# Kernel tuning notes

Measured on AMD Instinct MI355X. Metric: run time of the kernel, lower is better.

## Reference

```python
import jax, jax.numpy as jnp
import numpy as np

# dims: batch, samples, agents, obs_dim, action_dim, hidden
B, S, N, D, A, H = 512, 64, 8, 64, 16, 256
IN_DIM = (D + A) * N  # 640


def mish(x):
    return x * jnp.tanh(jax.nn.softplus(x))


def setup_inputs() -> dict:
    key = jax.random.key(0)
    ks = jax.random.split(key, 9)
    u = lambda k, shape, fan_in: jax.random.uniform(
        k, shape, jnp.float32, -1.0 / np.sqrt(fan_in), 1.0 / np.sqrt(fan_in))
    return {
        "state": jax.random.normal(ks[0], (B, N, D), jnp.float32),
        "action": jax.random.normal(ks[1], (B, N, A), jnp.float32),
        "W1": u(ks[2], (IN_DIM, H), IN_DIM),
        "b1": u(ks[3], (H,), IN_DIM),
        "W2": u(ks[4], (H, H), H),
        "b2": u(ks[5], (H,), H),
        "W3": u(ks[6], (H, 1), H),
        "b3": u(ks[7], (1,), H),
        # random grand-coalition permutations of the N agents, per (batch, sample)
        "perm": jnp.argsort(jax.random.uniform(ks[8], (B, S, N)), axis=-1).astype(jnp.int32),
    }


def reference(state, action, W1, b1, W2, b2, W3, b3, perm):
    # subcoalition mask [B,S,N,N]: torch builds one-hot(perm) @ tril(ones),
    # i.e. mask[b,s,i,j] = 1 iff j <= perm[b,s,i]
    subcoal = (jnp.arange(N) <= perm[..., None]).astype(state.dtype)
    # gathered actions in coalition order [B,S,N,A]: act_g[b,s,j] = action[b, perm[b,s,j]]
    act_g = action[jnp.arange(B)[:, None, None], perm]
    # masked subcoalition actions [B,S,N,N,A] -> [B,S,N,N*A]
    act = (act_g[:, :, None, :, :] * subcoal[..., None]).reshape(B, S, N, N * A)
    # flattened global obs broadcast over (sample, agent) axes [B,S,N,N*D]
    obs = jnp.broadcast_to(state.reshape(B, 1, 1, N * D), (B, S, N, N * D))
    x = jnp.concatenate([obs, act], axis=-1)  # [B,S,N,IN_DIM]
    # per-agent loop in torch uses shared q1 weights -> single batched MLP
    h = mish(x @ W1 + b1)
    h = mish(h @ W2 + b2)
    q = h @ W3 + b3                   # [B,S,N,1]
    q1 = q.mean(axis=1).squeeze(-1)   # mean over samples -> [B,N]
    return (q1, q1)
```

## Files before the change

kernel.cpp:

```cpp
#include <hip/hip_runtime.h>
#include <hip/hip_bf16.h>

typedef unsigned short ushort_t;
typedef __attribute__((ext_vector_type(8))) short short8;
typedef __attribute__((ext_vector_type(4))) float floatx4;


__device__ __forceinline__ float mish_f(float x) {
    float e = __expf(x);
    float w = fmaf(e, e + 2.0f, 2.0f);
    return x - 2.0f * x * __builtin_amdgcn_rcpf(w);
}

__device__ __forceinline__ unsigned f2bf_u(float f) {
    return (__float_as_uint(f) + 0x8000u) >> 16;
}

__device__ __forceinline__ unsigned pk_bf2(float a, float b) {
    unsigned ua = __float_as_uint(a) + 0x8000u;
    unsigned ub = __float_as_uint(b) + 0x8000u;
#if __has_builtin(__builtin_amdgcn_perm)
    return __builtin_amdgcn_perm(ua, ub, 0x03020706u);
#else
    return (ua >> 16) | (ub & 0xffff0000u);
#endif
}

__global__ __launch_bounds__(256) void prep_kernel(
        const float* __restrict__ state,
        const float* __restrict__ action,
        const float* __restrict__ W1,
        const float* __restrict__ b1,
        const float* __restrict__ W2,
        float* __restrict__ obsW,
        ushort_t* __restrict__ actW,
        ushort_t* __restrict__ W2T) {
    int bid = blockIdx.x;
    int t = threadIdx.x;
    if (bid < 512) {
        int b = bid;
        const float* stp = state + (size_t)b * 512;
        const float* w1p = W1 + t;
        float a0 = 0.f, a1 = 0.f, a2 = 0.f, a3 = 0.f;
#pragma unroll 8
        for (int f = 0; f < 512; f += 4) {
            a0 = fmaf(stp[f + 0], w1p[(f + 0) * 256], a0);
            a1 = fmaf(stp[f + 1], w1p[(f + 1) * 256], a1);
            a2 = fmaf(stp[f + 2], w1p[(f + 2) * 256], a2);
            a3 = fmaf(stp[f + 3], w1p[(f + 3) * 256], a3);
        }
        obsW[b * 256 + t] = (a0 + a1) + (a2 + a3) + b1[t];
    } else if (bid < 1536) {
        int idx = bid - 512;
        int j = idx & 7;
        int b0 = (idx >> 3) * 4;
        const float* W1a = W1 + (size_t)(512 + j * 16) * 256;
        float wv[16];
#pragma unroll
        for (int a = 0; a < 16; ++a) wv[a] = W1a[a * 256 + t];
#pragma unroll
        for (int bb = 0; bb < 4; ++bb) {
            int b = b0 + bb;
            const float* acp = action + (size_t)b * 128;
            float acc[8];
#pragma unroll
            for (int n = 0; n < 8; ++n) acc[n] = 0.f;
#pragma unroll
            for (int a = 0; a < 16; ++a) {
#pragma unroll
                for (int n = 0; n < 8; ++n)
                    acc[n] = fmaf(acp[n * 16 + a], wv[a], acc[n]);
            }
#pragma unroll
            for (int n = 0; n < 8; ++n)
                actW[(((size_t)b * 8 + n) * 8 + j) * 256 + t] = (ushort_t)f2bf_u(acc[n]);
        }
    } else {
        int n = (bid - 1536) * 4 + (t >> 6);
        int klo = (t & 63);
        for (int kk = 0; kk < 4; ++kk) {
            int k = kk * 64 + klo;
            W2T[n * 256 + k] = (ushort_t)f2bf_u(W2[k * 256 + n]);
        }
    }
}

#define CHUNK_US 528

__global__ __launch_bounds__(512, 4) void main_kernel(
        const float* __restrict__ obsW, const ushort_t* __restrict__ actW,
        const ushort_t* __restrict__ W2T, const int* __restrict__ perm,
        const float* __restrict__ b2,
        const float* __restrict__ W3, const float* __restrict__ b3,
        float* __restrict__ out) {
    __shared__ __align__(16) ushort_t h1[32 * CHUNK_US];
    __shared__ __align__(16) float obsb[256];
    __shared__ int perm_s[64];
    __shared__ float qpart[8][64];
    __shared__ float qv_s[64];

    int t = threadIdx.x;
    int bid = blockIdx.x;
    int b = (bid & 7) * 64 + ((bid >> 3) & 63);
    int sg = bid >> 9;
    int s0 = sg * 8;

    int w = t >> 6;
    int L = t & 63;
    int lo = L & 15;
    int q = L >> 4;

    if (t < 256) obsb[t] = obsW[b * 256 + t];
    else if (t < 320) perm_s[t - 256] = perm[((size_t)b * 64 + s0) * 8 + (t - 256)];

    const ushort_t* w2base = W2T + ((size_t)(w * 32 + lo)) * 256 + q * 8;
    short8 bpre[4];
    bpre[0] = *reinterpret_cast<const short8*>(w2base + 0 * 16 * 256 + 0 * 32);
    bpre[1] = *reinterpret_cast<const short8*>(w2base + 1 * 16 * 256 + 0 * 32);
    bpre[2] = *reinterpret_cast<const short8*>(w2base + 0 * 16 * 256 + 1 * 32);
    bpre[3] = *reinterpret_cast<const short8*>(w2base + 1 * 16 * 256 + 1 * 32);

    __syncthreads();

    {
        int sl = w;
        int hg = L;
        int g = hg >> 1;
        int ks = g >> 2;
        int qq = g & 3;
        int half = hg & 1;
        const ushort_t* actg = actW + (size_t)b * 64 * 256 + hg * 4;
        uint2 av[8];
#pragma unroll
        for (int j = 0; j < 8; ++j) {
            int p = perm_s[sl * 8 + j];
            av[j] = *reinterpret_cast<const uint2*>(actg + (p * 8 + j) * 256);
        }
        float4 ob = *reinterpret_cast<const float4*>(obsb + hg * 4);
        float r0 = ob.x, r1 = ob.y, r2 = ob.z, r3 = ob.w;
        ushort_t* dst0 = h1 + (qq * 16) * 8 + half * 4 + ks * CHUNK_US;
#pragma unroll
        for (int j = 0; j < 8; ++j) {
            r0 += __uint_as_float(av[j].x << 16);
            r1 += __uint_as_float(av[j].x & 0xffff0000u);
            r2 += __uint_as_float(av[j].y << 16);
            r3 += __uint_as_float(av[j].y & 0xffff0000u);
            int row = sl * 8 + j;
            int mt = row >> 4, lr = row & 15;
            uint2 pk = make_uint2(pk_bf2(mish_f(r0), mish_f(r1)),
                                  pk_bf2(mish_f(r2), mish_f(r3)));
            *reinterpret_cast<uint2*>(dst0 + mt * 8 * CHUNK_US + lr * 8) = pk;
        }
    }
    __syncthreads();

    floatx4 acc[4][2];
#pragma unroll
    for (int mt = 0; mt < 4; ++mt)
#pragma unroll
        for (int nt = 0; nt < 2; ++nt)
            acc[mt][nt] = (floatx4){0.f, 0.f, 0.f, 0.f};

    const ushort_t* h1b = h1 + L * 8;

#pragma unroll
    for (int ks = 0; ks < 8; ++ks) {
        short8 afr[4];
#pragma unroll
        for (int mt = 0; mt < 4; ++mt)
            afr[mt] = *reinterpret_cast<const short8*>(h1b + (mt * 8 + ks) * CHUNK_US);
#pragma unroll
        for (int nt = 0; nt < 2; ++nt) {
            short8 bfr;
            if (ks == 0)      bfr = bpre[nt];
            else if (ks == 1) bfr = bpre[2 + nt];
            else              bfr = *reinterpret_cast<const short8*>(w2base + nt * 16 * 256 + ks * 32);
#pragma unroll
            for (int mt = 0; mt < 4; ++mt)
                acc[mt][nt] = __builtin_amdgcn_mfma_f32_16x16x32_bf16(afr[mt], bfr, acc[mt][nt], 0, 0, 0);
        }
    }

    float b2c[2], w3c[2];
#pragma unroll
    for (int nt = 0; nt < 2; ++nt) {
        int col = w * 32 + nt * 16 + lo;
        b2c[nt] = b2[col];
        w3c[nt] = W3[col];
    }
#pragma unroll
    for (int mt = 0; mt < 4; ++mt) {
        float part[4] = {0.f, 0.f, 0.f, 0.f};
#pragma unroll
        for (int nt = 0; nt < 2; ++nt) {
#pragma unroll
            for (int r = 0; r < 4; ++r) {
                float h2 = mish_f(acc[mt][nt][r] + b2c[nt]);
                part[r] = fmaf(h2, w3c[nt], part[r]);
            }
        }
#pragma unroll
        for (int r = 0; r < 4; ++r) {
            float v = part[r];
            v += __shfl_xor(v, 1);
            v += __shfl_xor(v, 2);
            v += __shfl_xor(v, 4);
            v += __shfl_xor(v, 8);
            if (lo == 0) qpart[w][mt * 16 + q * 4 + r] = v;
        }
    }
    __syncthreads();
    if (t < 64) {
        float qv = b3[0];
#pragma unroll
        for (int ww = 0; ww < 8; ++ww) qv += qpart[ww][t];
        qv_s[t] = qv;
    }
    __syncthreads();
    if (t < 8) {
        float p = 0.f;
#pragma unroll
        for (int sl = 0; sl < 8; ++sl)
            p += qv_s[sl * 8 + perm_s[sl * 8 + t]];
        p *= (1.0f / 64.0f);
        atomicAdd(&out[b * 8 + t], p);
        atomicAdd(&out[4096 + b * 8 + t], p);
    }
}

extern "C" void kernel_launch(void* const* d_in, const int* in_sizes, int n_in,
                              void* d_out, int out_size, void* d_ws, size_t ws_size,
                              hipStream_t stream) {
    const float* state  = (const float*)d_in[0];
    const float* action = (const float*)d_in[1];
    const float* W1     = (const float*)d_in[2];
    const float* b1     = (const float*)d_in[3];
    const float* W2     = (const float*)d_in[4];
    const float* b2     = (const float*)d_in[5];
    const float* W3     = (const float*)d_in[6];
    const float* b3     = (const float*)d_in[7];
    const int*   perm   = (const int*)d_in[8];
    float* out = (float*)d_out;

    char* ws = (char*)d_ws;
    float*    obsW = (float*)ws;
    ushort_t* actW = (ushort_t*)(ws + 524288);
    ushort_t* W2T  = (ushort_t*)(ws + 524288 + 16777216);

    (void)hipMemsetAsync(out, 0, (size_t)out_size * sizeof(float), stream);
    prep_kernel<<<1600, 256, 0, stream>>>(state, action, W1, b1, W2, obsW, actW, W2T);
    main_kernel<<<4096, 512, 0, stream>>>(obsW, actW, W2T, perm, b2, W3, b3, out);
}
```

Measured before the change: 184.4 us.

## Switch to fp16 MFMA with exp2-prescaled mish, DPP reductions, fused output zeroing

Intermediates and W2 are now stored as fp16 instead of bf16, and the layer-2 matmul uses f16 MFMA. Pre-activations are pre-scaled by log2(e) so mish can use exp2 directly in a packed float2 form. The W3 dot product uses fdot2 and the 16-lane reductions use DPP instead of shuffles. The output memset is folded into the prep kernel and the prep grid is rebalanced. fp16 has narrower range than bf16, which could overflow, and fp16 rounding of h2 and W3 adds error.

```diff
diff --git a/kernel.cpp b/kernel.cpp
--- a/kernel.cpp
+++ b/kernel.cpp
@@ -2,28 +2,49 @@
 #include <hip/hip_bf16.h>
 
 typedef unsigned short ushort_t;
-typedef __attribute__((ext_vector_type(8))) short short8;
+typedef _Float16 half_t;
+typedef __attribute__((ext_vector_type(2))) _Float16 half2_t;
+typedef __attribute__((ext_vector_type(8))) _Float16 half8_t;
+typedef __attribute__((ext_vector_type(2))) float fx2;
 typedef __attribute__((ext_vector_type(4))) float floatx4;
 
-
-__device__ __forceinline__ float mish_f(float x) {
-    float e = __expf(x);
-    float w = fmaf(e, e + 2.0f, 2.0f);
-    return x - 2.0f * x * __builtin_amdgcn_rcpf(w);
-}
-
-__device__ __forceinline__ unsigned f2bf_u(float f) {
-    return (__float_as_uint(f) + 0x8000u) >> 16;
-}
-
-__device__ __forceinline__ unsigned pk_bf2(float a, float b) {
-    unsigned ua = __float_as_uint(a) + 0x8000u;
-    unsigned ub = __float_as_uint(b) + 0x8000u;
-#if __has_builtin(__builtin_amdgcn_perm)
-    return __builtin_amdgcn_perm(ua, ub, 0x03020706u);
+#define LOG2E 1.4426950408889634f
+#define LN2   0.6931471805599453f
+
+__device__ __forceinline__ float exp2_(float x) {
+#if __has_builtin(__builtin_amdgcn_exp2f)
+    return __builtin_amdgcn_exp2f(x);
 #else
-    return (ua >> 16) | (ub & 0xffff0000u);
+    return exp2f(x);
 #endif
+}
+
+__device__ __forceinline__ half2_t cvt_pk_f16(float a, float b) {
+    auto r = __builtin_amdgcn_cvt_pkrtz(a, b);
+    return __builtin_bit_cast(half2_t, r);
+}
+
+__device__ __forceinline__ fx2 mish2(fx2 t0) {
+    fx2 one = {1.0f, 1.0f};
+    fx2 m2  = {-2.0f, -2.0f};
+    fx2 u   = {exp2_(t0.x), exp2_(t0.y)};
+    fx2 s   = u + one;
+    fx2 wv  = __builtin_elementwise_fma(s, s, one);
+    fx2 rr  = {__builtin_amdgcn_rcpf(wv.x), __builtin_amdgcn_rcpf(wv.y)};
+    fx2 v   = __builtin_elementwise_fma(rr, m2, one);
+    return t0 * v;
+}
+
+__device__ __forceinline__ float dpp_sum16(float v) {
+    int x = __float_as_int(v);
+    v += __int_as_float(__builtin_amdgcn_update_dpp(0, x, 0xB1, 0xF, 0xF, true));
+    x = __float_as_int(v);
+    v += __int_as_float(__builtin_amdgcn_update_dpp(0, x, 0x4E, 0xF, 0xF, true));
+    x = __float_as_int(v);
+    v += __int_as_float(__builtin_amdgcn_update_dpp(0, x, 0x124, 0xF, 0xF, true));
+    x = __float_as_int(v);
+    v += __int_as_float(__builtin_amdgcn_update_dpp(0, x, 0x128, 0xF, 0xF, true));
+    return v;
 }
 
 __global__ __launch_bounds__(256) void prep_kernel(
@@ -33,8 +54,9 @@
         const float* __restrict__ b1,
         const float* __restrict__ W2,
         float* __restrict__ obsW,
-        ushort_t* __restrict__ actW,
-        ushort_t* __restrict__ W2T) {
+        half_t* __restrict__ actW,
+        half_t* __restrict__ W2T,
+        float* __restrict__ out) {
     int bid = blockIdx.x;
     int t = threadIdx.x;
     if (bid < 512) {
@@ -49,17 +71,17 @@
             a2 = fmaf(stp[f + 2], w1p[(f + 2) * 256], a2);
             a3 = fmaf(stp[f + 3], w1p[(f + 3) * 256], a3);
         }
-        obsW[b * 256 + t] = (a0 + a1) + (a2 + a3) + b1[t];
-    } else if (bid < 1536) {
+        obsW[b * 256 + t] = ((a0 + a1) + (a2 + a3) + b1[t]) * LOG2E;
+    } else if (bid < 2560) {
         int idx = bid - 512;
         int j = idx & 7;
-        int b0 = (idx >> 3) * 4;
+        int b0 = (idx >> 3) * 2;
         const float* W1a = W1 + (size_t)(512 + j * 16) * 256;
         float wv[16];
 #pragma unroll
         for (int a = 0; a < 16; ++a) wv[a] = W1a[a * 256 + t];
 #pragma unroll
-        for (int bb = 0; bb < 4; ++bb) {
+        for (int bb = 0; bb < 2; ++bb) {
             int b = b0 + bb;
             const float* acp = action + (size_t)b * 128;
             float acc[8];
@@ -73,14 +95,20 @@
             }
 #pragma unroll
             for (int n = 0; n < 8; ++n)
-                actW[(((size_t)b * 8 + n) * 8 + j) * 256 + t] = (ushort_t)f2bf_u(acc[n]);
+                actW[(((size_t)b * 8 + n) * 8 + j) * 256 + t] = (half_t)(acc[n] * LOG2E);
         }
     } else {
-        int n = (bid - 1536) * 4 + (t >> 6);
-        int klo = (t & 63);
-        for (int kk = 0; kk < 4; ++kk) {
-            int k = kk * 64 + klo;
-            W2T[n * 256 + k] = (ushort_t)f2bf_u(W2[k * 256 + n]);
+        int blk = bid - 2560;
+        if (blk < 16) {
+            out[blk * 512 + t] = 0.0f;
+            out[blk * 512 + 256 + t] = 0.0f;
+        }
+        int n = blk * 8 + (t >> 5);
+        int klo = t & 31;
+#pragma unroll
+        for (int kk = 0; kk < 8; ++kk) {
+            int k = kk * 32 + klo;
+            W2T[n * 256 + k] = (half_t)W2[k * 256 + n];
         }
     }
 }
@@ -88,8 +116,8 @@
 #define CHUNK_US 528
 
 __global__ __launch_bounds__(512, 4) void main_kernel(
-        const float* __restrict__ obsW, const ushort_t* __restrict__ actW,
-        const ushort_t* __restrict__ W2T, const int* __restrict__ perm,
+        const float* __restrict__ obsW, const half_t* __restrict__ actW,
+        const half_t* __restrict__ W2T, const int* __restrict__ perm,
         const float* __restrict__ b2,
         const float* __restrict__ W3, const float* __restrict__ b3,
         float* __restrict__ out) {
@@ -113,12 +141,12 @@
     if (t < 256) obsb[t] = obsW[b * 256 + t];
     else if (t < 320) perm_s[t - 256] = perm[((size_t)b * 64 + s0) * 8 + (t - 256)];
 
-    const ushort_t* w2base = W2T + ((size_t)(w * 32 + lo)) * 256 + q * 8;
-    short8 bpre[4];
-    bpre[0] = *reinterpret_cast<const short8*>(w2base + 0 * 16 * 256 + 0 * 32);
-    bpre[1] = *reinterpret_cast<const short8*>(w2base + 1 * 16 * 256 + 0 * 32);
-    bpre[2] = *reinterpret_cast<const short8*>(w2base + 0 * 16 * 256 + 1 * 32);
-    bpre[3] = *reinterpret_cast<const short8*>(w2base + 1 * 16 * 256 + 1 * 32);
+    const half_t* w2base = W2T + ((size_t)(w * 32 + lo)) * 256 + q * 8;
+    half8_t bpre[4];
+    bpre[0] = *reinterpret_cast<const half8_t*>(w2base + 0 * 16 * 256 + 0 * 32);
+    bpre[1] = *reinterpret_cast<const half8_t*>(w2base + 1 * 16 * 256 + 0 * 32);
+    bpre[2] = *reinterpret_cast<const half8_t*>(w2base + 0 * 16 * 256 + 1 * 32);
+    bpre[3] = *reinterpret_cast<const half8_t*>(w2base + 1 * 16 * 256 + 1 * 32);
 
     __syncthreads();
 
@@ -129,7 +157,7 @@
         int ks = g >> 2;
         int qq = g & 3;
         int half = hg & 1;
-        const ushort_t* actg = actW + (size_t)b * 64 * 256 + hg * 4;
+        const half_t* actg = actW + (size_t)b * 64 * 256 + hg * 4;
         uint2 av[8];
 #pragma unroll
         for (int j = 0; j < 8; ++j) {
@@ -137,18 +165,23 @@
             av[j] = *reinterpret_cast<const uint2*>(actg + (p * 8 + j) * 256);
         }
         float4 ob = *reinterpret_cast<const float4*>(obsb + hg * 4);
-        float r0 = ob.x, r1 = ob.y, r2 = ob.z, r3 = ob.w;
+        fx2 r01 = {ob.x, ob.y};
+        fx2 r23 = {ob.z, ob.w};
         ushort_t* dst0 = h1 + (qq * 16) * 8 + half * 4 + ks * CHUNK_US;
 #pragma unroll
         for (int j = 0; j < 8; ++j) {
-            r0 += __uint_as_float(av[j].x << 16);
-            r1 += __uint_as_float(av[j].x & 0xffff0000u);
-            r2 += __uint_as_float(av[j].y << 16);
-            r3 += __uint_as_float(av[j].y & 0xffff0000u);
+            half2_t a0 = __builtin_bit_cast(half2_t, av[j].x);
+            half2_t a1 = __builtin_bit_cast(half2_t, av[j].y);
+            r01 += (fx2){(float)a0.x, (float)a0.y};
+            r23 += (fx2){(float)a1.x, (float)a1.y};
+            fx2 h01 = mish2(r01);
+            fx2 h23 = mish2(r23);
+            half2_t p0 = cvt_pk_f16(h01.x, h01.y);
+            half2_t p1 = cvt_pk_f16(h23.x, h23.y);
             int row = sl * 8 + j;
             int mt = row >> 4, lr = row & 15;
-            uint2 pk = make_uint2(pk_bf2(mish_f(r0), mish_f(r1)),
-                                  pk_bf2(mish_f(r2), mish_f(r3)));
+            uint2 pk = make_uint2(__builtin_bit_cast(unsigned, p0),
+                                  __builtin_bit_cast(unsigned, p1));
             *reinterpret_cast<uint2*>(dst0 + mt * 8 * CHUNK_US + lr * 8) = pk;
         }
     }
@@ -165,47 +198,46 @@
 
 #pragma unroll
     for (int ks = 0; ks < 8; ++ks) {
-        short8 afr[4];
+        half8_t afr[4];
 #pragma unroll
         for (int mt = 0; mt < 4; ++mt)
-            afr[mt] = *reinterpret_cast<const short8*>(h1b + (mt * 8 + ks) * CHUNK_US);
+            afr[mt] = *reinterpret_cast<const half8_t*>(h1b + (mt * 8 + ks) * CHUNK_US);
 #pragma unroll
         for (int nt = 0; nt < 2; ++nt) {
-            short8 bfr;
+            half8_t bfr;
             if (ks == 0)      bfr = bpre[nt];
             else if (ks == 1) bfr = bpre[2 + nt];
-            else              bfr = *reinterpret_cast<const short8*>(w2base + nt * 16 * 256 + ks * 32);
+            else              bfr = *reinterpret_cast<const half8_t*>(w2base + nt * 16 * 256 + ks * 32);
 #pragma unroll
             for (int mt = 0; mt < 4; ++mt)
-                acc[mt][nt] = __builtin_amdgcn_mfma_f32_16x16x32_bf16(afr[mt], bfr, acc[mt][nt], 0, 0, 0);
-        }
-    }
-
-    float b2c[2], w3c[2];
-#pragma unroll
-    for (int nt = 0; nt < 2; ++nt) {
-        int col = w * 32 + nt * 16 + lo;
-        b2c[nt] = b2[col];
-        w3c[nt] = W3[col];
-    }
+                acc[mt][nt] = __builtin_amdgcn_mfma_f32_16x16x32_f16(afr[mt], bfr, acc[mt][nt], 0, 0, 0);
+        }
+    }
+
+    int col0 = w * 32 + 0 * 16 + lo;
+    int col1 = w * 32 + 1 * 16 + lo;
+    fx2 b2p = {b2[col0] * LOG2E, b2[col1] * LOG2E};
+    half2_t w3p = cvt_pk_f16(W3[col0] * LN2, W3[col1] * LN2);
 #pragma unroll
     for (int mt = 0; mt < 4; ++mt) {
-        float part[4] = {0.f, 0.f, 0.f, 0.f};
-#pragma unroll
-        for (int nt = 0; nt < 2; ++nt) {
-#pragma unroll
-            for (int r = 0; r < 4; ++r) {
-                float h2 = mish_f(acc[mt][nt][r] + b2c[nt]);
-                part[r] = fmaf(h2, w3c[nt], part[r]);
-            }
-        }
+        float part[4];
 #pragma unroll
         for (int r = 0; r < 4; ++r) {
-            float v = part[r];
-            v += __shfl_xor(v, 1);
-            v += __shfl_xor(v, 2);
-            v += __shfl_xor(v, 4);
-            v += __shfl_xor(v, 8);
+            fx2 t2 = {acc[mt][0][r], acc[mt][1][r]};
+            t2 += b2p;
+            fx2 h = mish2(t2);
+            half2_t hh = cvt_pk_f16(h.x, h.y);
+#if __has_builtin(__builtin_amdgcn_fdot2)
+            part[r] = __builtin_amdgcn_fdot2(__builtin_bit_cast(__fp16 __attribute__((ext_vector_type(2))), hh),
+                                             __builtin_bit_cast(__fp16 __attribute__((ext_vector_type(2))), w3p),
+                                             0.0f, false);
+#else
+            part[r] = (float)hh.x * (float)w3p.x + (float)hh.y * (float)w3p.y;
+#endif
+        }
+#pragma unroll
+        for (int r = 0; r < 4; ++r) {
+            float v = dpp_sum16(part[r]);
             if (lo == 0) qpart[w][mt * 16 + q * 4 + r] = v;
         }
     }
@@ -243,11 +275,10 @@
     float* out = (float*)d_out;
 
     char* ws = (char*)d_ws;
-    float*    obsW = (float*)ws;
-    ushort_t* actW = (ushort_t*)(ws + 524288);
-    ushort_t* W2T  = (ushort_t*)(ws + 524288 + 16777216);
-
-    (void)hipMemsetAsync(out, 0, (size_t)out_size * sizeof(float), stream);
-    prep_kernel<<<1600, 256, 0, stream>>>(state, action, W1, b1, W2, obsW, actW, W2T);
+    float*  obsW = (float*)ws;
+    half_t* actW = (half_t*)(ws + 524288);
+    half_t* W2T  = (half_t*)(ws + 524288 + 16777216);
+
+    prep_kernel<<<2592, 256, 0, stream>>>(state, action, W1, b1, W2, obsW, actW, W2T, out);
     main_kernel<<<4096, 512, 0, stream>>>(obsW, actW, W2T, perm, b2, W3, b3, out);
 }
```

New measurement: 178.3 us. 1.03x faster.
